# Kernel optimization log

Measured on AMD Instinct MI355X. Metric: run time of the kernel, lower is better.

The kernel has to match this reference:

```python
import jax, jax.numpy as jnp
import numpy as np
from jax import lax

B, IN_C, Q_C, V_C, H, W = 16, 3, 8, 16, 224, 224
K = 7  # static conv kernel size


def _conv(x, w, stride=2, pad=3):
    # x: [N, Cin, H, W], w: [Cout, Cin, kh, kw]
    return lax.conv_general_dilated(
        x, w, (stride, stride), [(pad, pad), (pad, pad)],
        dimension_numbers=("NCHW", "OIHW", "NCHW"))


def _dyn_conv(inp, w):
    # per-sample dynamic conv: inp [C, H, W], w [O, C, kh, kw] -> [O, oh, ow]
    return _conv(inp[None], w, stride=2, pad=3)[0]


def setup_inputs() -> dict:
    key = jax.random.key(0)
    ks = jax.random.split(key, 8)
    x = jax.random.normal(ks[0], (B, IN_C, H, W), dtype=jnp.float32)
    # q_conv_params: input_channel x (weight [q, in, 7, 7], bias [q])
    Wq = jax.random.normal(ks[1], (IN_C, Q_C, IN_C, K, K), dtype=jnp.float32)
    bq = jax.random.normal(ks[2], (IN_C, Q_C), dtype=jnp.float32)
    # k_conv_paramss: input_channel x v_channel x (weight [q, in, 7, 7], bias [q])
    Wk = jax.random.normal(ks[3], (IN_C, V_C, Q_C, IN_C, K, K), dtype=jnp.float32)
    bk = jax.random.normal(ks[4], (IN_C, V_C, Q_C), dtype=jnp.float32)
    # v_conv_param: (weight [v, in, 7, 7], bias [v])
    Wv = jax.random.normal(ks[5], (V_C, IN_C, K, K), dtype=jnp.float32)
    bv = jax.random.normal(ks[6], (V_C,), dtype=jnp.float32)
    return {"x": x, "Wq": Wq, "bq": bq, "Wk": Wk, "bk": bk, "Wv": Wv, "bv": bv}


def reference(x, Wq, bq, Wk, bk, Wv, bv):
    b = x.shape[0]
    in_c, q_c = Wq.shape[0], Wq.shape[1]
    v_c = Wk.shape[1]
    # q: stack of input_channel static convs -> one grouped-by-output conv
    q = _conv(x, Wq.reshape(in_c * q_c, *Wq.shape[2:])) \
        + bq.reshape(-1)[None, :, None, None]
    h2, w2 = q.shape[-2], q.shape[-1]  # 112, 112
    q = q.reshape(b, in_c, q_c, h2, w2)
    # ks: input_channel x v_channel static convs fused into one conv
    kmap = _conv(x, Wk.reshape(in_c * v_c * q_c, *Wk.shape[3:])) \
        + bk.reshape(-1)[None, :, None, None]
    kmap = kmap.reshape(b, in_c, v_c, q_c, h2, w2)
    # a: per (batch, in_c) dynamic conv with feature maps as 112x112 kernels
    # input q[b,i] [q_c, h2, w2], weight kmap[b,i] [v_c, q_c, h2, w2] -> [v_c, 4, 4]
    a = jax.vmap(jax.vmap(_dyn_conv))(q, kmap)  # [B, in_c, v_c, 4, 4]
    # v: static conv
    v = _conv(x, Wv) + bv[None, :, None, None]  # [B, v_c, h2, w2]
    # o: per-batch dynamic conv with a[b] as kernel -> [B, in_c, 58, 58]
    o = jax.vmap(_dyn_conv)(v, a)
    return o
```

## Files before the change

kernel.cpp:

```cpp
#include <hip/hip_runtime.h>
#include <hip/hip_bf16.h>

#define BATCH 16
#define IN_C 3
#define Q_C 8
#define V_C 16
#define HH 224
#define WW 224
#define KK 7

#define XPH 230
#define XPW 232
#define QPH 118
#define QPW 120
#define QP_PLANE (QPH*QPW)
#define QP_QSTRIDE (Q_C*QP_PLANE)

#define PT_MB    202
#define PT2_CHUNKS (BATCH*IN_C*PT_MB*112)
#define PT2_N    ((size_t)PT2_CHUNKS*8)

#define PLANES_N (BATCH*7*IN_C*XPH*QPW)
#define VPAD_N   (BATCH*V_C*QPH*QPW)
#define QPADS_N  (BATCH*IN_C*QP_QSTRIDE)
#define D_N      (BATCH*160*384)
#define SPLITS   16
#define DPART_N  (SPLITS*D_N)
#define OUT_N    (BATCH*IN_C*58*58)
#define AW_N     (4*48*192)

typedef __attribute__((ext_vector_type(8))) short bf16x8;
typedef __attribute__((ext_vector_type(4))) float f32x4;
typedef __attribute__((ext_vector_type(4))) unsigned short u16x4;

struct __attribute__((packed, aligned(4))) uint4_a4 { uint4 v; };

static __device__ inline unsigned short f2b(float f) {
    __hip_bfloat16 h = __float2bfloat16(f);
    return *reinterpret_cast<unsigned short*>(&h);
}
static __device__ inline float b2f(unsigned short u) {
    unsigned int v = ((unsigned int)u) << 16;
    return __builtin_bit_cast(float, v);
}
static __device__ inline bf16x8 ld16(const unsigned short* p) {
    return __builtin_bit_cast(bf16x8, *(const uint4*)p);
}

__global__ __launch_bounds__(256) void kXT(const float* __restrict__ x,
                                           unsigned short* __restrict__ planes,
                                           unsigned short* __restrict__ pT2) {
    int blk = blockIdx.x;
    int r0 = blk % 29;
    int t0 = blk / 29;
    int ci = t0 % IN_C;
    int b  = t0 / IN_C;
    int tid = threadIdx.x;

    __shared__ unsigned short xl[8][240];

    const float* xb = x + (size_t)(b * IN_C + ci) * (HH * WW);
    for (int idx = tid; idx < 8 * 240; idx += 256) {
        int row8 = idx / 240, c = idx % 240;
        int r = 8 * r0 + row8 - 3;
        int cc = c - 3;
        float val = 0.0f;
        if (r >= 0 && r < HH && cc >= 0 && cc < WW)
            val = xb[(size_t)r * WW + cc];
        xl[row8][c] = f2b(val);
    }
    __syncthreads();

    for (int t2 = tid; t2 < 784; t2 += 256) {
        int ko = t2 % 14;
        int t3 = t2 / 14;
        int row8 = t3 % 8;
        int dx = t3 / 8;
        int prow = 8 * r0 + row8;
        if (prow >= XPH) continue;
        unsigned short pk[8];
        #pragma unroll
        for (int j = 0; j < 8; ++j)
            pk[j] = xl[row8][16 * ko + 2 * j + dx];
        unsigned short* dst = planes
            + ((size_t)((b * 7 + dx) * IN_C + ci) * XPH + prow) * QPW + 8 * ko;
        *(uint4*)dst = *(const uint4*)pk;
    }

    for (int t2 = tid; t2 < 784; t2 += 256) {
        int kc  = t2 % 112;
        int mbr = t2 / 112;
        int mb = 7 * r0 + mbr;
        if (mb >= PT_MB) continue;
        unsigned short pk[8];
        #pragma unroll
        for (int j = 0; j < 8; ++j) {
            int mrel = 8 * mbr + j;
            int row8 = mrel / 7;
            int dxm  = mrel - 7 * row8;
            pk[j] = xl[row8][2 * kc + dxm];
        }
        unsigned short* dst = pT2 + ((size_t)((b * IN_C + ci) * PT_MB + mb) * 112 + kc) * 8;
        *(uint4*)dst = *(const uint4*)pk;
    }
}

__global__ __launch_bounds__(256) void kW(const float* __restrict__ Wq,
                                          const float* __restrict__ Wv,
                                          unsigned short* __restrict__ Aw2) {
    int idx = blockIdx.x * 256 + threadIdx.x;
    if (idx >= AW_N) return;
    int n = idx % 192;
    int t3 = idx / 192;
    int ch = t3 % 48;
    int p4 = t3 / 48;
    int ci = n / 64;
    int t  = (n % 64) - 2 * p4;
    float v = 0.0f;
    if (ch < 40 && t >= 0 && t < 49) {
        int k = ci * 49 + t;
        v = (ch < 24) ? Wq[(size_t)ch * 147 + k] : Wv[(size_t)(ch - 24) * 147 + k];
    }
    Aw2[idx] = f2b(v);
}

__global__ __launch_bounds__(256) void kA(const unsigned short* __restrict__ pT2,
                                          const unsigned short* __restrict__ Aw2,
                                          const float* __restrict__ bq,
                                          const float* __restrict__ bv,
                                          unsigned short* __restrict__ qpadS,
                                          float* __restrict__ vpad) {
    int g = blockIdx.x;
    int r8 = g & 7, q8 = g >> 3;
    int b  = r8 + 8 * (q8 / 28);
    int yq = q8 % 28;
    int w  = threadIdx.x >> 6;
    int yo = yq * 4 + w;
    int lane = threadIdx.x & 63;
    int cl = lane & 15, kq = lane >> 4;

    int m14 = 14 * yo;
    int p4  = (m14 >> 1) & 3;
    int ms8 = m14 >> 3;

    const unsigned short* AwP = Aw2 + (size_t)p4 * (48 * 192);
    bf16x8 af[3][6];
    #pragma unroll
    for (int mt = 0; mt < 3; ++mt)
        #pragma unroll
        for (int s = 0; s < 6; ++s)
            af[mt][s] = ld16(AwP + (size_t)(mt * 16 + cl) * 192 + s * 32 + kq * 8);

    f32x4 acc[3][7];
    #pragma unroll
    for (int mt = 0; mt < 3; ++mt)
        #pragma unroll
        for (int nt = 0; nt < 7; ++nt)
            acc[mt][nt] = f32x4{0.f, 0.f, 0.f, 0.f};

    #pragma unroll
    for (int s = 0; s < 6; ++s) {
        int ci = s >> 1;
        int mb = ms8 + kq + 4 * (s & 1);
        const unsigned short* bp = pT2
            + ((size_t)((b * IN_C + ci) * PT_MB + mb) * 112) * 8;
        bf16x8 bfr[7];
        #pragma unroll
        for (int nt = 0; nt < 7; ++nt)
            bfr[nt] = ld16(bp + (size_t)(nt * 16 + cl) * 8);
        #pragma unroll
        for (int nt = 0; nt < 7; ++nt)
            #pragma unroll
            for (int mt = 0; mt < 3; ++mt)
                acc[mt][nt] = __builtin_amdgcn_mfma_f32_16x16x32_bf16(af[mt][s], bfr[nt], acc[mt][nt], 0, 0, 0);
    }

    float bias[3][4];
    #pragma unroll
    for (int mt = 0; mt < 3; ++mt)
        #pragma unroll
        for (int r = 0; r < 4; ++r) {
            int ch = mt * 16 + kq * 4 + r;
            bias[mt][r] = (ch < 24) ? bq[ch] : (ch < 40 ? bv[ch - 24] : 0.0f);
        }

    int orow = yo + 3;
    #pragma unroll
    for (int mt = 0; mt < 3; ++mt) {
        #pragma unroll
        for (int nt = 0; nt < 7; ++nt) {
            int kc = nt * 16 + cl;
            #pragma unroll
            for (int r = 0; r < 4; ++r) {
                int ch = mt * 16 + kq * 4 + r;
                float val = acc[mt][nt][r] + bias[mt][r];
                if (ch < 24) {
                    qpadS[((size_t)(b * 3 + (ch >> 3)) * 8 + (ch & 7)) * QP_PLANE
                          + (size_t)orow * QPW + 3 + kc] = f2b(val);
                } else if (ch < 40) {
                    vpad[((size_t)(b * 16 + (ch - 24)) * QPH + orow) * QPW + 3 + kc] = val;
                }
            }
        }
    }
}

__global__ __launch_bounds__(512, 4) void kC(const unsigned short* __restrict__ planes,
                                             const unsigned short* __restrict__ qpadS,
                                             unsigned short* __restrict__ Dpart) {
    int blk = blockIdx.x;
    int b   = blk & 15;
    int nh  = (blk >> 4) & 1;
    int yc  = blk >> 5;
    int tid = threadIdx.x;
    int w = tid >> 6, lane = tid & 63;
    int tt = lane & 15, kq = lane >> 4;
    int th = tt >> 2, tw = tt & 3;

    __shared__ union {
        uint4 bs[2][80 * 17];
        unsigned short dq[40 * 392];
    } sm;

    int nreal = nh ? 67 : 80;

    if (tid < nreal * 3) {
        int nl = tid / 3, j2 = tid % 3;
        sm.bs[0][nl * 17 + 14 + j2] = uint4{0, 0, 0, 0};
        sm.bs[1][nl * 17 + 14 + j2] = uint4{0, 0, 0, 0};
    } else if (nh == 1) {
        int t2 = tid - nreal * 3;
        if (t2 < 13 * 17) {
            int nl = 67 + t2 / 17, ss = t2 % 17;
            uint4 v = (ss < 14) ? uint4{0x3F803F80u, 0x3F803F80u, 0x3F803F80u, 0x3F803F80u}
                                : uint4{0, 0, 0, 0};
            sm.bs[0][nl * 17 + ss] = v;
            sm.bs[1][nl * 17 + ss] = v;
        }
    }

    int nch = nreal * 14;
    int soff[3];
    int sdst[3];
    bool sact[3];
    #pragma unroll
    for (int i = 0; i < 3; ++i) {
        int c = tid + 512 * i;
        sact[i] = (c < nch);
        int cc2 = sact[i] ? c : 0;
        int nl = cc2 / 14;
        int k0 = (cc2 % 14) * 8;
        int n = nh * 80 + nl;
        int ci = n / 49;
        int rr = n % 49;
        int dy = rr / 7;
        int dx = rr % 7;
        soff[i] = (((b * 7 + dx) * IN_C + ci) * XPH + dy) * QPW + k0;
        sdst[i] = nl * 17 + (k0 >> 3);
    }

    const unsigned short* abase[3];
    #pragma unroll
    for (int j = 0; j < 3; ++j) {
        int tile = w * 3 + j;
        int ic = tile >> 3, qc = tile & 7;
        abase[j] = qpadS + (size_t)(b * IN_C + ic) * QP_QSTRIDE + qc * QP_PLANE
                 + (2 * th) * QPW + 2 * tw;
    }

    f32x4 acc[3][5];
    #pragma unroll
    for (int j = 0; j < 3; ++j)
        #pragma unroll
        for (int nt = 0; nt < 5; ++nt)
            acc[j][nt] = f32x4{0.f, 0.f, 0.f, 0.f};

    int yo0 = yc * 7;
    #pragma unroll
    for (int i = 0; i < 3; ++i)
        if (sact[i]) sm.bs[0][sdst[i]] = *(const uint4*)(planes + soff[i] + yo0 * 240);
    uint4 pf[3];
    #pragma unroll
    for (int i = 0; i < 3; ++i)
        if (sact[i]) pf[i] = *(const uint4*)(planes + soff[i] + (yo0 + 1) * 240);
    __syncthreads();

    for (int ry = 0; ry < 7; ++ry) {
        int yo = yo0 + ry;
        int cur = ry & 1;
        if (ry < 6) {
            #pragma unroll
            for (int i = 0; i < 3; ++i)
                if (sact[i]) sm.bs[cur ^ 1][sdst[i]] = pf[i];
        }
        if (ry < 5) {
            #pragma unroll
            for (int i = 0; i < 3; ++i)
                if (sact[i]) pf[i] = *(const uint4*)(planes + soff[i] + (yo + 2) * 240);
        }
        #pragma unroll
        for (int s = 0; s < 4; ++s) {
            int k = 32 * s + kq * 8;
            int xs = (k < 112) ? k : 96;
            bf16x8 af[3];
            #pragma unroll
            for (int j = 0; j < 3; ++j)
                af[j] = __builtin_bit_cast(bf16x8,
                    ((const uint4_a4*)(abase[j] + yo * QPW + xs))->v);
            #pragma unroll
            for (int nt = 0; nt < 5; ++nt) {
                bf16x8 bf = __builtin_bit_cast(bf16x8, sm.bs[cur][(nt * 16 + tt) * 17 + 4 * s + kq]);
                #pragma unroll
                for (int j = 0; j < 3; ++j)
                    acc[j][nt] = __builtin_amdgcn_mfma_f32_16x16x32_bf16(af[j], bf, acc[j][nt], 0, 0, 0);
            }
        }
        __syncthreads();
    }

    unsigned short* Dp = Dpart + (size_t)(yc * 16 + b) * (160 * 384);
    #pragma unroll
    for (int pass = 0; pass < 2; ++pass) {
        if (pass) __syncthreads();
        #pragma unroll
        for (int j = 0; j < 3; ++j) {
            int tile = w * 3 + j;
            int mb = tile * 16 + kq * 4;
            #pragma unroll
            for (int nt = 0; nt < 5; ++nt) {
                int nl = nt * 16 + tt;
                int hi = (nl >= 40) ? 1 : 0;
                if (hi == pass) {
                    u16x4 pk;
                    pk.x = f2b(acc[j][nt][0]);
                    pk.y = f2b(acc[j][nt][1]);
                    pk.z = f2b(acc[j][nt][2]);
                    pk.w = f2b(acc[j][nt][3]);
                    *(u16x4*)(&sm.dq[(nl - pass * 40) * 392 + mb]) = pk;
                }
            }
        }
        __syncthreads();
        for (int c = tid; c < 40 * 48; c += 512) {
            int nl = c / 48, ms = c % 48;
            *(uint4*)(Dp + (size_t)(nh * 80 + pass * 40 + nl) * 384 + ms * 8) =
                *(const uint4*)(&sm.dq[nl * 392 + ms * 8]);
        }
    }
}

__global__ __launch_bounds__(256) void kR(const unsigned short* __restrict__ Dpart,
                                          float* __restrict__ Df) {
    int idx = blockIdx.x * 256 + threadIdx.x;
    float4 s = float4{0.f, 0.f, 0.f, 0.f};
    #pragma unroll
    for (int yc = 0; yc < SPLITS; ++yc) {
        u16x4 v = *(const u16x4*)(Dpart + (size_t)yc * D_N + 4 * (size_t)idx);
        s.x += b2f(v.x);
        s.y += b2f(v.y);
        s.z += b2f(v.z);
        s.w += b2f(v.w);
    }
    *(float4*)(Df + 4 * (size_t)idx) = s;
}

__global__ __launch_bounds__(256) void kE(const float* __restrict__ Df,
                                          const float* __restrict__ Wk,
                                          const float* __restrict__ bk,
                                          float* __restrict__ a_out) {
    int blk = blockIdx.x;
    int bi = blk >> 4;
    int v  = blk & 15;
    int ic = bi % IN_C;
    int b  = bi / IN_C;
    int tid = threadIdx.x;
    int t  = tid & 15;
    int rl = tid >> 4;
    const float* Dbase = Df + (size_t)b * (160 * 384);
    const float* WkI = Wk + (size_t)(ic * V_C + v) * (Q_C * 147);
    const float* bkI = bk + (ic * V_C + v) * Q_C;
    float s = 0.0f;
    for (int qc = 0; qc < Q_C; ++qc) {
        const float* wrow = WkI + qc * 147;
        int mcol = ic * 128 + qc * 16 + t;
        #pragma unroll
        for (int j = 0; j < 10; ++j) {
            int r = rl + 16 * j;
            if (r < 148) {
                float wv = (r < 147) ? wrow[r] : bkI[qc];
                s = fmaf(wv, Dbase[(size_t)r * 384 + mcol], s);
            }
        }
    }
    __shared__ float red[256];
    red[tid] = s;
    __syncthreads();
    if (tid < 16) {
        float acc2 = 0.f;
        #pragma unroll
        for (int k2 = 0; k2 < 16; ++k2) acc2 += red[k2 * 16 + tid];
        a_out[(size_t)blk * 16 + tid] = acc2;
    }
}

__global__ __launch_bounds__(256) void kO(const float* __restrict__ vpad,
                                          const float* __restrict__ a,
                                          float* __restrict__ out) {
    int idx = blockIdx.x * 256 + threadIdx.x;
    if (idx >= OUT_N) return;
    int ow = idx % 58;
    int t = idx / 58;
    int oh = t % 58; t /= 58;
    int ic = t % IN_C;
    int b  = t / IN_C;
    const float* ab = a + (size_t)(b * IN_C + ic) * (V_C * 16);
    float s = 0.0f;
    for (int vc = 0; vc < V_C; ++vc) {
        const float* vrow = vpad + ((size_t)(b * V_C + vc) * QPH + 2 * oh) * QPW + 2 * ow;
        const float* ar = ab + vc * 16;
        #pragma unroll
        for (int kh = 0; kh < 4; ++kh)
            #pragma unroll
            for (int kw = 0; kw < 4; ++kw)
                s = fmaf(vrow[kh * QPW + kw], ar[kh * 4 + kw], s);
    }
    out[idx] = s;
}

extern "C" void kernel_launch(void* const* d_in, const int* in_sizes, int n_in,
                              void* d_out, int out_size, void* d_ws, size_t ws_size,
                              hipStream_t stream) {
    (void)in_sizes; (void)n_in; (void)out_size; (void)ws_size;
    const float* x  = (const float*)d_in[0];
    const float* Wq = (const float*)d_in[1];
    const float* bq = (const float*)d_in[2];
    const float* Wk = (const float*)d_in[3];
    const float* bk = (const float*)d_in[4];
    const float* Wv = (const float*)d_in[5];
    const float* bv = (const float*)d_in[6];
    float* out = (float*)d_out;

    char* p = (char*)d_ws;
    unsigned short* pT2   = (unsigned short*)p;
    unsigned short* Dpart = (unsigned short*)p;
    p += (size_t)DPART_N * 2;
    unsigned short* planes = (unsigned short*)p;        p += (size_t)PLANES_N * 2;
    float*          vpad   = (float*)p;                 p += (size_t)VPAD_N * 4;
    unsigned short* qpadS  = (unsigned short*)p;        p += (size_t)QPADS_N * 2;
    float*          Df     = (float*)p;                 p += (size_t)D_N * 4;
    unsigned short* Aw2    = (unsigned short*)p;        p += (size_t)AW_N * 2;
    float*          a      = (float*)p;

    kXT<<<BATCH * IN_C * 29, 256, 0, stream>>>(x, planes, pT2);
    kW<<<(AW_N + 255) / 256, 256, 0, stream>>>(Wq, Wv, Aw2);
    hipMemsetAsync(vpad, 0, (size_t)VPAD_N * 4 + (size_t)QPADS_N * 2, stream);
    kA<<<448, 256, 0, stream>>>(pT2, Aw2, bq, bv, qpadS, vpad);
    kC<<<SPLITS * 2 * 16, 512, 0, stream>>>(planes, qpadS, Dpart);
    kR<<<D_N / 4 / 256, 256, 0, stream>>>(Dpart, Df);
    kE<<<BATCH * IN_C * V_C, 256, 0, stream>>>(Df, Wk, bk, a);
    kO<<<(OUT_N + 255) / 256, 256, 0, stream>>>(vpad, a, out);
}
```

Before: 188.7 us.

## Replace full memset with border zeroing, stage kA stores in LDS, retile kO

The full-buffer memset of the padded q/v maps is replaced by a small kernel that zeroes only the top and bottom padding rows. kA now stages each output row in shared memory, including the left and right pad columns, and writes it back with coalesced 16-byte stores instead of scattered scalar stores. kC drops its double-buffered B tile for a single buffer with two barriers per step, and writes the D partials back in one pass instead of two. kO caches the dynamic kernel `a` in shared memory per (batch, channel) block and uses float2 loads, at the cost of a much smaller grid.

```diff
diff --git a/kernel.cpp b/kernel.cpp
--- a/kernel.cpp
+++ b/kernel.cpp
@@ -28,6 +28,9 @@
 #define DPART_N  (SPLITS*D_N)
 #define OUT_N    (BATCH*IN_C*58*58)
 #define AW_N     (4*48*192)
+
+#define ZQ_CHUNKS (BATCH*IN_C*Q_C*6*15)
+#define ZV_CHUNKS (BATCH*V_C*6*30)
 
 typedef __attribute__((ext_vector_type(8))) short bf16x8;
 typedef __attribute__((ext_vector_type(4))) float f32x4;
@@ -71,17 +74,22 @@
     }
     __syncthreads();
 
-    for (int t2 = tid; t2 < 784; t2 += 256) {
-        int ko = t2 % 14;
-        int t3 = t2 / 14;
+    for (int t2 = tid; t2 < 840; t2 += 256) {
+        int ko = t2 % 15;
+        int t3 = t2 / 15;
         int row8 = t3 % 8;
         int dx = t3 / 8;
         int prow = 8 * r0 + row8;
         if (prow >= XPH) continue;
         unsigned short pk[8];
-        #pragma unroll
-        for (int j = 0; j < 8; ++j)
-            pk[j] = xl[row8][16 * ko + 2 * j + dx];
+        if (ko < 14) {
+            #pragma unroll
+            for (int j = 0; j < 8; ++j)
+                pk[j] = xl[row8][16 * ko + 2 * j + dx];
+        } else {
+            #pragma unroll
+            for (int j = 0; j < 8; ++j) pk[j] = 0;
+        }
         unsigned short* dst = planes
             + ((size_t)((b * 7 + dx) * IN_C + ci) * XPH + prow) * QPW + 8 * ko;
         *(uint4*)dst = *(const uint4*)pk;
@@ -124,6 +132,29 @@
     Aw2[idx] = f2b(v);
 }
 
+__global__ __launch_bounds__(256) void kZ(unsigned short* __restrict__ qpadS,
+                                          float* __restrict__ vpad) {
+    int idx = blockIdx.x * 256 + threadIdx.x;
+    if (idx >= ZQ_CHUNKS + ZV_CHUNKS) return;
+    uint4 z = uint4{0, 0, 0, 0};
+    if (idx < ZQ_CHUNKS) {
+        int ko = idx % 15;
+        int t2 = idx / 15;
+        int r6 = t2 % 6;
+        int plane = t2 / 6;
+        int row = (r6 < 3) ? r6 : (112 + r6);
+        *(uint4*)(qpadS + (size_t)plane * QP_PLANE + (size_t)row * QPW + 8 * ko) = z;
+    } else {
+        int j = idx - ZQ_CHUNKS;
+        int ko = j % 30;
+        int t2 = j / 30;
+        int r6 = t2 % 6;
+        int plane = t2 / 6;
+        int row = (r6 < 3) ? r6 : (112 + r6);
+        *(uint4*)((char*)(vpad + (size_t)plane * QP_PLANE + (size_t)row * QPW) + 16 * ko) = z;
+    }
+}
+
 __global__ __launch_bounds__(256) void kA(const unsigned short* __restrict__ pT2,
                                           const unsigned short* __restrict__ Aw2,
                                           const float* __restrict__ bq,
@@ -139,6 +170,9 @@
     int lane = threadIdx.x & 63;
     int cl = lane & 15, kq = lane >> 4;
 
+    __shared__ unsigned short qs[4][24][120];
+    __shared__ float          vs[4][16][120];
+
     int m14 = 14 * yo;
     int p4  = (m14 >> 1) & 3;
     int ms8 = m14 >> 3;
@@ -184,7 +218,15 @@
             bias[mt][r] = (ch < 24) ? bq[ch] : (ch < 40 ? bv[ch - 24] : 0.0f);
         }
 
-    int orow = yo + 3;
+    for (int i = lane; i < 24 * 8; i += 64) {
+        int ch = i / 8, c = i % 8;
+        qs[w][ch][(c < 3) ? c : (112 + c)] = 0;
+    }
+    for (int i = lane; i < 16 * 8; i += 64) {
+        int ch = i / 8, c = i % 8;
+        vs[w][ch][(c < 3) ? c : (112 + c)] = 0.0f;
+    }
+
     #pragma unroll
     for (int mt = 0; mt < 3; ++mt) {
         #pragma unroll
@@ -194,14 +236,25 @@
             for (int r = 0; r < 4; ++r) {
                 int ch = mt * 16 + kq * 4 + r;
                 float val = acc[mt][nt][r] + bias[mt][r];
-                if (ch < 24) {
-                    qpadS[((size_t)(b * 3 + (ch >> 3)) * 8 + (ch & 7)) * QP_PLANE
-                          + (size_t)orow * QPW + 3 + kc] = f2b(val);
-                } else if (ch < 40) {
-                    vpad[((size_t)(b * 16 + (ch - 24)) * QPH + orow) * QPW + 3 + kc] = val;
-                }
+                if (ch < 24) qs[w][ch][3 + kc] = f2b(val);
+                else if (ch < 40) vs[w][ch - 24][3 + kc] = val;
             }
         }
+    }
+    __syncthreads();
+
+    int orow = yo + 3;
+    for (int i = lane; i < 24 * 15; i += 64) {
+        int ch = i / 15, ko = i % 15;
+        int icq = ch >> 3, qc = ch & 7;
+        *(uint4*)(qpadS + (size_t)((b * 3 + icq) * 8 + qc) * QP_PLANE
+                  + (size_t)orow * QPW + 8 * ko) = *(const uint4*)(&qs[w][ch][8 * ko]);
+    }
+    for (int i = lane; i < 16 * 30; i += 64) {
+        int ch = i / 30, ko = i % 30;
+        *(float4*)((char*)(vpad + (size_t)(b * 16 + ch) * QP_PLANE
+                           + (size_t)orow * QPW) + 16 * ko) =
+            *(const float4*)((const char*)(&vs[w][ch][0]) + 16 * ko);
     }
 }
 
@@ -218,24 +271,22 @@
     int th = tt >> 2, tw = tt & 3;
 
     __shared__ union {
-        uint4 bs[2][80 * 17];
-        unsigned short dq[40 * 392];
+        uint4 bs[80 * 17];
+        unsigned short dq[80 * 392];
     } sm;
 
     int nreal = nh ? 67 : 80;
 
     if (tid < nreal * 3) {
         int nl = tid / 3, j2 = tid % 3;
-        sm.bs[0][nl * 17 + 14 + j2] = uint4{0, 0, 0, 0};
-        sm.bs[1][nl * 17 + 14 + j2] = uint4{0, 0, 0, 0};
+        sm.bs[nl * 17 + 14 + j2] = uint4{0, 0, 0, 0};
     } else if (nh == 1) {
         int t2 = tid - nreal * 3;
         if (t2 < 13 * 17) {
             int nl = 67 + t2 / 17, ss = t2 % 17;
             uint4 v = (ss < 14) ? uint4{0x3F803F80u, 0x3F803F80u, 0x3F803F80u, 0x3F803F80u}
                                 : uint4{0, 0, 0, 0};
-            sm.bs[0][nl * 17 + ss] = v;
-            sm.bs[1][nl * 17 + ss] = v;
+            sm.bs[nl * 17 + ss] = v;
         }
     }
 
@@ -275,28 +326,23 @@
         for (int nt = 0; nt < 5; ++nt)
             acc[j][nt] = f32x4{0.f, 0.f, 0.f, 0.f};
 
+    uint4 pf[3];
     int yo0 = yc * 7;
     #pragma unroll
     for (int i = 0; i < 3; ++i)
-        if (sact[i]) sm.bs[0][sdst[i]] = *(const uint4*)(planes + soff[i] + yo0 * 240);
-    uint4 pf[3];
-    #pragma unroll
-    for (int i = 0; i < 3; ++i)
-        if (sact[i]) pf[i] = *(const uint4*)(planes + soff[i] + (yo0 + 1) * 240);
-    __syncthreads();
+        if (sact[i]) pf[i] = *(const uint4*)(planes + soff[i] + yo0 * 240);
 
     for (int ry = 0; ry < 7; ++ry) {
-        int yo = yo0 + ry;
-        int cur = ry & 1;
+        int yo = yc * 7 + ry;
+        __syncthreads();
+        #pragma unroll
+        for (int i = 0; i < 3; ++i)
+            if (sact[i]) sm.bs[sdst[i]] = pf[i];
+        __syncthreads();
         if (ry < 6) {
             #pragma unroll
             for (int i = 0; i < 3; ++i)
-                if (sact[i]) sm.bs[cur ^ 1][sdst[i]] = pf[i];
-        }
-        if (ry < 5) {
-            #pragma unroll
-            for (int i = 0; i < 3; ++i)
-                if (sact[i]) pf[i] = *(const uint4*)(planes + soff[i] + (yo + 2) * 240);
+                if (sact[i]) pf[i] = *(const uint4*)(planes + soff[i] + (yo + 1) * 240);
         }
         #pragma unroll
         for (int s = 0; s < 4; ++s) {
@@ -309,43 +355,36 @@
                     ((const uint4_a4*)(abase[j] + yo * QPW + xs))->v);
             #pragma unroll
             for (int nt = 0; nt < 5; ++nt) {
-                bf16x8 bf = __builtin_bit_cast(bf16x8, sm.bs[cur][(nt * 16 + tt) * 17 + 4 * s + kq]);
+                bf16x8 bf = __builtin_bit_cast(bf16x8, sm.bs[(nt * 16 + tt) * 17 + 4 * s + kq]);
                 #pragma unroll
                 for (int j = 0; j < 3; ++j)
                     acc[j][nt] = __builtin_amdgcn_mfma_f32_16x16x32_bf16(af[j], bf, acc[j][nt], 0, 0, 0);
             }
         }
-        __syncthreads();
-    }
-
+    }
+
+    __syncthreads();
+    #pragma unroll
+    for (int j = 0; j < 3; ++j) {
+        int tile = w * 3 + j;
+        int mb = tile * 16 + kq * 4;
+        #pragma unroll
+        for (int nt = 0; nt < 5; ++nt) {
+            int nl = nt * 16 + tt;
+            u16x4 pk;
+            pk.x = f2b(acc[j][nt][0]);
+            pk.y = f2b(acc[j][nt][1]);
+            pk.z = f2b(acc[j][nt][2]);
+            pk.w = f2b(acc[j][nt][3]);
+            *(u16x4*)(&sm.dq[nl * 392 + mb]) = pk;
+        }
+    }
+    __syncthreads();
     unsigned short* Dp = Dpart + (size_t)(yc * 16 + b) * (160 * 384);
-    #pragma unroll
-    for (int pass = 0; pass < 2; ++pass) {
-        if (pass) __syncthreads();
-        #pragma unroll
-        for (int j = 0; j < 3; ++j) {
-            int tile = w * 3 + j;
-            int mb = tile * 16 + kq * 4;
-            #pragma unroll
-            for (int nt = 0; nt < 5; ++nt) {
-                int nl = nt * 16 + tt;
-                int hi = (nl >= 40) ? 1 : 0;
-                if (hi == pass) {
-                    u16x4 pk;
-                    pk.x = f2b(acc[j][nt][0]);
-                    pk.y = f2b(acc[j][nt][1]);
-                    pk.z = f2b(acc[j][nt][2]);
-                    pk.w = f2b(acc[j][nt][3]);
-                    *(u16x4*)(&sm.dq[(nl - pass * 40) * 392 + mb]) = pk;
-                }
-            }
-        }
-        __syncthreads();
-        for (int c = tid; c < 40 * 48; c += 512) {
-            int nl = c / 48, ms = c % 48;
-            *(uint4*)(Dp + (size_t)(nh * 80 + pass * 40 + nl) * 384 + ms * 8) =
-                *(const uint4*)(&sm.dq[nl * 392 + ms * 8]);
-        }
+    for (int c = tid; c < 80 * 48; c += 512) {
+        int nl = c / 48, ms = c % 48;
+        *(uint4*)(Dp + (size_t)(nh * 80 + nl) * 384 + ms * 8) =
+            *(const uint4*)(&sm.dq[nl * 392 + ms * 8]);
     }
 }
 
@@ -406,25 +445,36 @@
 __global__ __launch_bounds__(256) void kO(const float* __restrict__ vpad,
                                           const float* __restrict__ a,
                                           float* __restrict__ out) {
-    int idx = blockIdx.x * 256 + threadIdx.x;
-    if (idx >= OUT_N) return;
-    int ow = idx % 58;
-    int t = idx / 58;
-    int oh = t % 58; t /= 58;
-    int ic = t % IN_C;
-    int b  = t / IN_C;
-    const float* ab = a + (size_t)(b * IN_C + ic) * (V_C * 16);
-    float s = 0.0f;
-    for (int vc = 0; vc < V_C; ++vc) {
-        const float* vrow = vpad + ((size_t)(b * V_C + vc) * QPH + 2 * oh) * QPW + 2 * ow;
-        const float* ar = ab + vc * 16;
-        #pragma unroll
-        for (int kh = 0; kh < 4; ++kh)
-            #pragma unroll
-            for (int kw = 0; kw < 4; ++kw)
-                s = fmaf(vrow[kh * QPW + kw], ar[kh * 4 + kw], s);
-    }
-    out[idx] = s;
+    int blk = blockIdx.x;
+    int quarter = blk / 48, rem = blk % 48;
+    int b = rem % 16, ic = rem / 16;
+
+    __shared__ float as[256];
+    as[threadIdx.x] = a[(size_t)(b * 3 + ic) * 256 + threadIdx.x];
+    __syncthreads();
+
+    const float* vb = vpad + (size_t)b * 16 * QP_PLANE;
+    int p0 = quarter * 841;
+    for (int p = p0 + threadIdx.x; p < p0 + 841 && p < 3364; p += 256) {
+        int oh = p / 58, ow = p % 58;
+        float s = 0.0f;
+        #pragma unroll
+        for (int vc = 0; vc < 16; ++vc) {
+            const float* vrow = vb + ((size_t)vc * QPH + 2 * oh) * QPW + 2 * ow;
+            const float* ar = &as[vc * 16];
+            #pragma unroll
+            for (int kh = 0; kh < 4; ++kh) {
+                const float* vr = vrow + kh * QPW;
+                float2 x0 = *(const float2*)(vr);
+                float2 x1 = *(const float2*)(vr + 2);
+                s = fmaf(x0.x, ar[kh * 4 + 0], s);
+                s = fmaf(x0.y, ar[kh * 4 + 1], s);
+                s = fmaf(x1.x, ar[kh * 4 + 2], s);
+                s = fmaf(x1.y, ar[kh * 4 + 3], s);
+            }
+        }
+        out[(size_t)(b * 3 + ic) * 3364 + p] = s;
+    }
 }
 
 extern "C" void kernel_launch(void* const* d_in, const int* in_sizes, int n_in,
@@ -453,10 +503,10 @@
 
     kXT<<<BATCH * IN_C * 29, 256, 0, stream>>>(x, planes, pT2);
     kW<<<(AW_N + 255) / 256, 256, 0, stream>>>(Wq, Wv, Aw2);
-    hipMemsetAsync(vpad, 0, (size_t)VPAD_N * 4 + (size_t)QPADS_N * 2, stream);
+    kZ<<<(ZQ_CHUNKS + ZV_CHUNKS + 255) / 256, 256, 0, stream>>>(qpadS, vpad);
     kA<<<448, 256, 0, stream>>>(pT2, Aw2, bq, bv, qpadS, vpad);
     kC<<<SPLITS * 2 * 16, 512, 0, stream>>>(planes, qpadS, Dpart);
     kR<<<D_N / 4 / 256, 256, 0, stream>>>(Dpart, Df);
     kE<<<BATCH * IN_C * V_C, 256, 0, stream>>>(Df, Wk, bk, a);
-    kO<<<(OUT_N + 255) / 256, 256, 0, stream>>>(vpad, a, out);
-}
+    kO<<<192, 256, 0, stream>>>(vpad, a, out);
+}
```

Result: slower. 222.7 us (+18.0%).
